# Performance work log

Hardware: AMD Instinct MI355X
Metric: run time of the kernel (lower is better)

Reference implementation:

```python
import jax, jax.numpy as jnp
import numpy as np

DIM = 512
HID = 1024        # dim * expansion_factor
QK = 128          # query_key_dim
G = 256           # group_size
EPS = 1e-5


def setup_inputs() -> dict:
    key = jax.random.key(0)
    ks = jax.random.split(key, 6)
    x = jax.random.normal(ks[0], (4, 4096, DIM), jnp.float32)
    ln_w = jnp.ones((DIM,), jnp.float32)
    ln_b = jnp.zeros((DIM,), jnp.float32)
    Wh = 0.02 * jax.random.normal(ks[1], (DIM, 2 * HID), jnp.float32)
    bh = jnp.zeros((2 * HID,), jnp.float32)
    Wqk = 0.02 * jax.random.normal(ks[2], (DIM, QK), jnp.float32)
    bqk = jnp.zeros((QK,), jnp.float32)
    gamma = 0.02 * jax.random.normal(ks[3], (4, QK), jnp.float32)  # nn.init.normal_(gamma, std=0.02)
    beta = jnp.zeros((4, QK), jnp.float32)
    Wo = 0.02 * jax.random.normal(ks[4], (HID, DIM), jnp.float32)
    bo = jnp.zeros((DIM,), jnp.float32)
    return {"x": x, "ln_w": ln_w, "ln_b": ln_b, "Wh": Wh, "bh": bh,
            "Wqk": Wqk, "bqk": bqk, "gamma": gamma, "beta": beta,
            "Wo": Wo, "bo": bo}


def reference(x, ln_w, ln_b, Wh, bh, Wqk, bqk, gamma, beta, Wo, bo):
    b, n, _ = x.shape
    g = n // G  # number of groups (n chosen as multiple of G -> no padding)

    # LayerNorm (torch uses biased variance)
    mu = jnp.mean(x, axis=-1, keepdims=True)
    var = jnp.mean((x - mu) ** 2, axis=-1, keepdims=True)
    normed = (x - mu) * jax.lax.rsqrt(var + EPS) * ln_w + ln_b

    # to_hidden: Linear -> SiLU, split into v / gate
    h = jax.nn.silu(normed @ Wh + bh)            # [b, n, 2*HID]
    v, gate = jnp.split(h, 2, axis=-1)           # each [b, n, HID]

    # to_qk: Linear -> SiLU, then 4-head offset/scale
    qk = jax.nn.silu(normed @ Wqk + bqk)         # [b, n, QK]
    qkh = qk[..., None, :] * gamma + beta        # [b, n, 4, QK]
    quad_q, lin_q, quad_k, lin_k = (qkh[..., i, :] for i in range(4))

    # group: b (g n) d -> b g n d
    grp = lambda t: t.reshape(b, g, G, t.shape[-1])
    qq, qk_, lq, lk, vv = map(grp, (quad_q, quad_k, lin_q, lin_k, v))

    # quadratic (group-local) attention with ReLU^2 scores, causal within group
    sim = jnp.einsum('bgid,bgjd->bgij', qq, qk_) / G
    attn = jnp.square(jnp.maximum(sim, 0.0))
    causal_mask = jnp.triu(jnp.ones((G, G), dtype=bool), 1)
    attn = jnp.where(causal_mask, 0.0, attn)
    quad_out = jnp.einsum('bgij,bgje->bgie', attn, vv)   # [b, g, G, HID]

    # linear attention across groups: per-group kv, exclusive cumsum over group dim
    lin_kv = jnp.einsum('bgnd,bgne->bgde', lk, vv) / G   # [b, g, QK, HID]
    lin_kv = jnp.cumsum(lin_kv, axis=1)
    lin_kv = jnp.pad(lin_kv, ((0, 0), (1, 0), (0, 0), (0, 0)))[:, :-1]
    lin_out = jnp.einsum('bgde,bgnd->bgne', lin_kv, lq)  # [b, g, G, HID]

    out = gate * (quad_out.reshape(b, n, HID) + lin_out.reshape(b, n, HID))
    return out @ Wo + bo + x
```

## Files before the change

kernel.cpp:

```cpp
#include <hip/hip_runtime.h>
#include <hip/hip_bf16.h>
#include <math.h>


#define BATCH 4
#define SEQ   4096
#define TROWS 16384
#define DIMD  512
#define HIDD  1024
#define QKD   128
#define GRP   256
#define NGRP  16
#define BGRP  64
#define EPIW  132
#define EPB   130

typedef unsigned short bfraw;
typedef __attribute__((ext_vector_type(8))) short bf16x8;
typedef __attribute__((ext_vector_type(8))) unsigned short u16x8;
typedef __attribute__((ext_vector_type(4))) unsigned int u32x4;
typedef __attribute__((ext_vector_type(4))) float f32x4;

__device__ __forceinline__ float bf2f(bfraw u) {
    union { float f; unsigned int i; } c;
    c.i = ((unsigned int)u) << 16;
    return c.f;
}
__device__ __forceinline__ bfraw f2bf(float f) {
    unsigned int x = __float_as_uint(f);
    unsigned int r = (x + 0x7fffu + ((x >> 16) & 1u)) >> 16;
    return (bfraw)r;
}
__device__ __forceinline__ unsigned int pkbf(float lo, float hi) {
    __hip_bfloat162 h2 = __float22bfloat162_rn(make_float2(lo, hi));
    union { __hip_bfloat162 h; unsigned int u; } c; c.h = h2;
    return c.u;
}
__device__ __forceinline__ void store16bf(bfraw* dst, const float* src) {
    u32x4 a, b;
    #pragma unroll
    for (int k = 0; k < 4; ++k) a[k] = pkbf(src[2 * k], src[2 * k + 1]);
    #pragma unroll
    for (int k = 0; k < 4; ++k) b[k] = pkbf(src[8 + 2 * k], src[8 + 2 * k + 1]);
    *(u32x4*)dst = a;
    *(u32x4*)(dst + 8) = b;
}
__device__ __forceinline__ void store8bf(bfraw* dst, const float* src) {
    u32x4 a;
    #pragma unroll
    for (int k = 0; k < 4; ++k) a[k] = pkbf(src[2 * k], src[2 * k + 1]);
    *(u32x4*)dst = a;
}
__device__ __forceinline__ float silu_f(float z) {
    return z / (1.f + __expf(-z));
}
__device__ __forceinline__ void gload_lds16(const void* g, void* l) {
    __builtin_amdgcn_global_load_lds(
        (const __attribute__((address_space(1))) unsigned int*)g,
        (__attribute__((address_space(3))) unsigned int*)l, 16, 0, 0);
}

__device__ __forceinline__ void mfma_step(const bfraw* As, const bfraw* Bs,
                                          f32x4 acc[4][4], int wm, int wn,
                                          int q, int mi) {
    bf16x8 af[4], bfg[4];
    #pragma unroll
    for (int i = 0; i < 4; ++i)
        af[i] = *(const bf16x8*)&As[(size_t)(wm * 64 + i * 16 + mi) * 32 + q * 8];
    #pragma unroll
    for (int j = 0; j < 4; ++j)
        bfg[j] = *(const bf16x8*)&Bs[(size_t)(wn * 64 + j * 16 + mi) * 32 + q * 8];
    #pragma unroll
    for (int i = 0; i < 4; ++i)
        #pragma unroll
        for (int j = 0; j < 4; ++j)
            acc[i][j] = __builtin_amdgcn_mfma_f32_16x16x32_bf16(af[i], bfg[j], acc[i][j], 0, 0, 0);
}

#define SMEMP_DECL                                              \
    __shared__ __align__(16) char smem_[33280];                 \
    bfraw* A0buf = (bfraw*)smem_;                               \
    bfraw* B0buf = (bfraw*)(smem_ + 8192);                      \
    bfraw* A1buf = (bfraw*)(smem_ + 16384);                     \
    bfraw* B1buf = (bfraw*)(smem_ + 24576);

#define PIPE_DSTS                                               \
    bfraw* a0d  = A0buf + wid * 512;                            \
    bfraw* a0d2 = A0buf + 2048 + wid * 512;                     \
    bfraw* b0d  = B0buf + wid * 512;                            \
    bfraw* b0d2 = B0buf + 2048 + wid * 512;                     \
    bfraw* a1d  = A1buf + wid * 512;                            \
    bfraw* a1d2 = A1buf + 2048 + wid * 512;                     \
    bfraw* b1d  = B1buf + wid * 512;                            \
    bfraw* b1d2 = B1buf + 2048 + wid * 512;

#define KLOOP_PRE(Abase, Astr, Bbase, Bstr)                                    \
    const bfraw* pa0 = (Abase) + (size_t)(t >> 2) * (Astr) + (t & 3) * 8;      \
    const bfraw* pa1 = pa0 + (size_t)64 * (Astr);                              \
    const bfraw* pb0 = (Bbase) + (size_t)(t >> 2) * (Bstr) + (t & 3) * 8;      \
    const bfraw* pb1 = pb0 + (size_t)64 * (Bstr);

#define STAGE0                                                                 \
    do { gload_lds16(pa0, a0d); gload_lds16(pa1, a0d2);                        \
         gload_lds16(pb0, b0d); gload_lds16(pb1, b0d2);                        \
         pa0 += 32; pa1 += 32; pb0 += 32; pb1 += 32; } while (0)
#define STAGE1                                                                 \
    do { gload_lds16(pa0, a1d); gload_lds16(pa1, a1d2);                        \
         gload_lds16(pb0, b1d); gload_lds16(pb1, b1d2);                        \
         pa0 += 32; pa1 += 32; pb0 += 32; pb1 += 32; } while (0)

#define PIPE_LOOP(NIT, Abase, Astr, Bbase, Bstr)                               \
    {                                                                          \
        KLOOP_PRE(Abase, Astr, Bbase, Bstr)                                    \
        STAGE0;                                                                \
        for (int it = 0; it < (NIT); it += 2) {                                \
            __syncthreads();                                                   \
            if (it + 1 < (NIT)) STAGE1;                                        \
            mfma_step(A0buf, B0buf, acc, wm, wn, q, mi);                       \
            __syncthreads();                                                   \
            if (it + 2 < (NIT)) STAGE0;                                        \
            if (it + 1 < (NIT))                                                \
                mfma_step(A1buf, B1buf, acc, wm, wn, q, mi);                   \
        }                                                                      \
        __syncthreads();                                                       \
    }

__device__ __forceinline__ int epi_row(int p, int lr) {
    return (lr < 16) ? (p * 16 + lr) : (64 + p * 16 + (lr - 16));
}

__global__ __launch_bounds__(256) void prep_kernel(const float* __restrict__ x,
                                                   const float* __restrict__ lnw,
                                                   const float* __restrict__ lnb,
                                                   const float* __restrict__ Wh,
                                                   const float* __restrict__ Wo,
                                                   const float* __restrict__ Wqk,
                                                   bfraw* __restrict__ normb,
                                                   bfraw* __restrict__ WhT,
                                                   bfraw* __restrict__ WoT,
                                                   bfraw* __restrict__ WqkT) {
    __shared__ float tile[32][33];
    int bid = blockIdx.x;
    int t = threadIdx.x;
    if (bid < 4096) {
        int row  = bid * 4 + (t >> 6);
        int lane = t & 63;
        const float* xr = x + (size_t)row * DIMD;
        float4 v0 = ((const float4*)xr)[lane];
        float4 v1 = ((const float4*)xr)[lane + 64];
        float s  = v0.x + v0.y + v0.z + v0.w + v1.x + v1.y + v1.z + v1.w;
        float ss = v0.x*v0.x + v0.y*v0.y + v0.z*v0.z + v0.w*v0.w
                 + v1.x*v1.x + v1.y*v1.y + v1.z*v1.z + v1.w*v1.w;
        #pragma unroll
        for (int off = 32; off; off >>= 1) {
            s  += __shfl_xor(s, off);
            ss += __shfl_xor(ss, off);
        }
        float mu  = s * (1.f / DIMD);
        float var = ss * (1.f / DIMD) - mu * mu;
        float inv = rsqrtf(var + 1e-5f);
        float4 w0 = ((const float4*)lnw)[lane],  w1 = ((const float4*)lnw)[lane + 64];
        float4 b0 = ((const float4*)lnb)[lane],  b1 = ((const float4*)lnb)[lane + 64];
        unsigned int o0 = pkbf((v0.x - mu) * inv * w0.x + b0.x,
                               (v0.y - mu) * inv * w0.y + b0.y);
        unsigned int o1 = pkbf((v0.z - mu) * inv * w0.z + b0.z,
                               (v0.w - mu) * inv * w0.w + b0.w);
        unsigned int o2 = pkbf((v1.x - mu) * inv * w1.x + b1.x,
                               (v1.y - mu) * inv * w1.y + b1.y);
        unsigned int o3 = pkbf((v1.z - mu) * inv * w1.z + b1.z,
                               (v1.w - mu) * inv * w1.w + b1.w);
        unsigned int* brow = (unsigned int*)(normb + (size_t)row * DIMD);
        ((uint2*)brow)[lane]      = make_uint2(o0, o1);
        ((uint2*)brow)[lane + 64] = make_uint2(o2, o3);
        return;
    }
    bid -= 4096;
    const float* in; bfraw* outp; int R, C, nx;
    if (bid < 1024)      { in = Wh;  outp = WhT;  R = DIMD; C = 2 * HIDD; nx = 64; }
    else if (bid < 1536) { bid -= 1024; in = Wo;  outp = WoT;  R = HIDD; C = DIMD; nx = 16; }
    else                 { bid -= 1536; in = Wqk; outp = WqkT; R = DIMD; C = QKD;  nx = 4; }
    int c0 = (bid % nx) * 32, r0 = (bid / nx) * 32;
    int tr = t >> 3, tc4 = (t & 7) * 4;
    float4 v = *(const float4*)&in[(size_t)(r0 + tr) * C + c0 + tc4];
    tile[tr][tc4 + 0] = v.x; tile[tr][tc4 + 1] = v.y;
    tile[tr][tc4 + 2] = v.z; tile[tr][tc4 + 3] = v.w;
    __syncthreads();
    ushort4 s;
    s.x = f2bf(tile[tc4 + 0][tr]);
    s.y = f2bf(tile[tc4 + 1][tr]);
    s.z = f2bf(tile[tc4 + 2][tr]);
    s.w = f2bf(tile[tc4 + 3][tr]);
    *(ushort4*)&outp[(size_t)(c0 + tr) * R + r0 + tc4] = s;
}

__global__ __launch_bounds__(512, 4) void gemm_h256(
    const bfraw* __restrict__ A,
    const bfraw* __restrict__ WhT,
    const bfraw* __restrict__ WqkT,
    const float* __restrict__ bh,
    const float* __restrict__ bqk,
    const float* __restrict__ gamma,
    const float* __restrict__ beta,
    bfraw* __restrict__ vT,
    bfraw* __restrict__ gate,
    bfraw* __restrict__ qq,
    bfraw* __restrict__ lq,
    bfraw* __restrict__ kk,
    bfraw* __restrict__ lkT) {
    __shared__ __align__(16) char smem_[73728];
    const int t = threadIdx.x;
    const int lane = t & 63, wid = t >> 6;
    const int wm = wid >> 2, wn = wid & 3;
    const int q = lane >> 4, mi = lane & 15;
    int nid = (blockIdx.x & 7) * 144 + (blockIdx.x >> 3);
    const int ct = nid % 9, by = nid / 9;
    const int r0 = by * 128, c0 = ct * 256;
    const int bg = r0 >> 8;
    const int jb0 = r0 & 255;

    const int lslot = (t & 7) ^ ((t >> 3) & 7);
    const int srow  = 2 * (t >> 3) + (lslot >> 2);
    const int skel  = (lslot & 3) * 8;
    const bfraw* Asrc = A + (size_t)(r0 + srow) * DIMD + skel;
    const bfraw* Bsrc0;
    const bfraw* Bsrc1;
    if (ct < 8) {
        Bsrc0 = WhT + (size_t)(c0 + srow) * DIMD + skel;
        Bsrc1 = Bsrc0 + (size_t)128 * DIMD;
    } else {
        Bsrc0 = WqkT + (size_t)srow * DIMD + skel;
        Bsrc1 = Bsrc0;
    }
    const int swz = ((((mi & 1) << 2) | q) ^ ((mi >> 1) & 7)) << 4;
    const int a_off = (wm * 32 + (mi >> 1)) * 128 + swz;
    const int b_off = (wn * 32 + (mi >> 1)) * 128 + swz;

#define GH_STAGE(KT, SLOT)                                                    \
    do {                                                                      \
        char* sb_ = smem_ + (SLOT) * 24576;                                   \
        gload_lds16(Asrc  + (KT) * 32, sb_ + t * 16);                         \
        gload_lds16(Bsrc0 + (KT) * 32, sb_ + 8192 + t * 16);                  \
        gload_lds16(Bsrc1 + (KT) * 32, sb_ + 16384 + t * 16);                 \
    } while (0)

    f32x4 acc[4][4] = {};
    GH_STAGE(0, 0);
    GH_STAGE(1, 1);
    asm volatile("s_waitcnt vmcnt(3)" ::: "memory");
    __builtin_amdgcn_s_barrier();

    #pragma unroll
    for (int j = 0; j < 16; ++j) {
        if (j + 2 < 16) GH_STAGE(j + 2, (j + 2) % 3);
        const char* cb = smem_ + (j % 3) * 24576;
        bf16x8 af[4], bfr[4];
        #pragma unroll
        for (int mf = 0; mf < 4; ++mf)
            af[mf] = *(const bf16x8*)(cb + a_off + mf * 1024);
        #pragma unroll
        for (int nf = 0; nf < 4; ++nf)
            bfr[nf] = *(const bf16x8*)(cb + 8192 + b_off + nf * 1024);
        __builtin_amdgcn_s_setprio(1);
        #pragma unroll
        for (int mf = 0; mf < 4; ++mf)
            #pragma unroll
            for (int nf = 0; nf < 4; ++nf)
                acc[mf][nf] = __builtin_amdgcn_mfma_f32_16x16x32_bf16(
                    af[mf], bfr[nf], acc[mf][nf], 0, 0, 0);
        __builtin_amdgcn_s_setprio(0);
        if (j + 2 < 16)      asm volatile("s_waitcnt vmcnt(3)" ::: "memory");
        else if (j + 1 < 16) asm volatile("s_waitcnt vmcnt(0)" ::: "memory");
        __builtin_amdgcn_s_barrier();
    }
#undef GH_STAGE

    float* epi = (float*)smem_;
    if (ct == 8) {
        float* gbl = (float*)(smem_ + 36864);
        gbl[t] = gamma[t];
        gbl[t + 512] = beta[t];
        float bq4[4];
        #pragma unroll
        for (int nf = 0; nf < 4; ++nf)
            bq4[nf] = (wn < 2) ? bqk[wn * 64 + nf * 16 + mi] : 0.f;
        #pragma unroll
        for (int p2 = 0; p2 < 4; ++p2) {
            if (wm == (p2 >> 1) && wn < 2) {
                #pragma unroll
                for (int mf2 = 0; mf2 < 2; ++mf2) {
                    int mf = ((p2 & 1) << 1) + mf2;
                    #pragma unroll
                    for (int nf = 0; nf < 4; ++nf)
                        #pragma unroll
                        for (int rg = 0; rg < 4; ++rg)
                            epi[(mf2 * 16 + q * 4 + rg) * 132 + wn * 64 + nf * 16 + mi] =
                                silu_f(acc[mf][nf][rg] + bq4[nf]);
                }
            }
            __syncthreads();
            {
                int lr = t >> 4, cs = (t & 15) * 8;
                float z[8];
                #pragma unroll
                for (int k = 0; k < 8; ++k) z[k] = epi[lr * 132 + cs + k];
                size_t growr = (size_t)(r0 + p2 * 32 + lr) * QKD + cs;
                #pragma unroll
                for (int hd = 0; hd < 3; ++hd) {
                    bfraw* arr = (hd == 0) ? qq : (hd == 1) ? lq : kk;
                    float tmp[8];
                    #pragma unroll
                    for (int k = 0; k < 8; ++k)
                        tmp[k] = z[k] * gbl[hd * 128 + cs + k] + gbl[512 + hd * 128 + cs + k];
                    store8bf(arr + growr, tmp);
                }
            }
            {
                int c = t >> 2, jh = (t & 3) * 8;
                float g3 = gbl[384 + c], e3 = gbl[896 + c];
                float tmp[8];
                #pragma unroll
                for (int k = 0; k < 8; ++k)
                    tmp[k] = epi[(jh + k) * 132 + c] * g3 + e3;
                store8bf(lkT + ((size_t)bg * QKD + c) * GRP + jb0 + p2 * 32 + jh, tmp);
            }
            __syncthreads();
        }
        return;
    }
    float bias4[4];
    #pragma unroll
    for (int nf = 0; nf < 4; ++nf)
        bias4[nf] = bh[c0 + wn * 64 + nf * 16 + mi];
    if (ct < 4) {
        #pragma unroll
        for (int p2 = 0; p2 < 4; ++p2) {
            if (wm == (p2 >> 1)) {
                #pragma unroll
                for (int mf2 = 0; mf2 < 2; ++mf2) {
                    int mf = ((p2 & 1) << 1) + mf2;
                    #pragma unroll
                    for (int nf = 0; nf < 4; ++nf)
                        #pragma unroll
                        for (int rg = 0; rg < 4; ++rg)
                            epi[(mf2 * 16 + q * 4 + rg) * 257 + wn * 64 + nf * 16 + mi] =
                                silu_f(acc[mf][nf][rg] + bias4[nf]);
                }
            }
            __syncthreads();
            int e2 = t >> 1, js = (t & 1) * 16;
            float tmp[16];
            #pragma unroll
            for (int k = 0; k < 16; ++k)
                tmp[k] = epi[(js + k) * 257 + e2];
            store16bf(vT + ((size_t)bg * HIDD + c0 + e2) * GRP + jb0 + p2 * 32 + js, tmp);
            __syncthreads();
        }
    } else {
        #pragma unroll
        for (int p2 = 0; p2 < 4; ++p2) {
            if (wm == (p2 >> 1)) {
                #pragma unroll
                for (int mf2 = 0; mf2 < 2; ++mf2) {
                    int mf = ((p2 & 1) << 1) + mf2;
                    #pragma unroll
                    for (int nf = 0; nf < 4; ++nf)
                        #pragma unroll
                        for (int rg = 0; rg < 4; ++rg)
                            epi[(mf2 * 16 + q * 4 + rg) * 260 + wn * 64 + nf * 16 + mi] =
                                silu_f(acc[mf][nf][rg] + bias4[nf]);
                }
            }
            __syncthreads();
            int lr = t >> 4, cs = (t & 15) * 16;
            float tmp[16];
            #pragma unroll
            for (int k = 0; k < 16; ++k)
                tmp[k] = epi[lr * 260 + cs + k];
            store16bf(gate + (size_t)(r0 + p2 * 32 + lr) * HIDD + (c0 - HIDD) + cs, tmp);
            __syncthreads();
        }
    }
}

__global__ __launch_bounds__(256) void simkv_kernel(const bfraw* __restrict__ qq,
                                                    const bfraw* __restrict__ kk,
                                                    bfraw* __restrict__ attn,
                                                    const bfraw* __restrict__ vT,
                                                    const bfraw* __restrict__ lkT,
                                                    bfraw* __restrict__ kvT_raw) {
    SMEMP_DECL
    float* epi = (float*)smem_;
    int t = threadIdx.x;
    int lane = t & 63, wid = t >> 6;
    int wm = wid >> 1, wn = wid & 1;
    int q = lane >> 4, mi = lane & 15;
    int bid = blockIdx.x;
    f32x4 acc[4][4] = {};
    PIPE_DSTS
    if (bid < 512) {
        int bg = bid >> 3;
        int row0 = (bid & 7) * 128;
        PIPE_LOOP(8, vT + (size_t)bg * HIDD * GRP + (size_t)row0 * GRP, GRP,
                  lkT + (size_t)bg * QKD * GRP, GRP)
        bfraw* outg = kvT_raw + (size_t)bg * HIDD * QKD;
        #pragma unroll
        for (int p = 0; p < 4; ++p) {
            #pragma unroll
            for (int j = 0; j < 4; ++j)
                #pragma unroll
                for (int rg = 0; rg < 4; ++rg)
                    epi[(wm * 16 + q * 4 + rg) * EPIW + wn * 64 + j * 16 + mi] = acc[p][j][rg];
            __syncthreads();
            int lr = t >> 3, c0t = (t & 7) * 16;
            int gr = row0 + epi_row(p, lr);
            store16bf(outg + (size_t)gr * QKD + c0t, &epi[lr * EPIW + c0t]);
            __syncthreads();
        }
        return;
    }
    int i = bid - 512;
    int bg = i & 63;
    int tid = i >> 6;
    int ry = (tid == 0) ? 0 : 1;
    int rx = (tid == 2) ? 1 : 0;
    int row0 = ry * 128, col0 = rx * 128;
    PIPE_LOOP(4, qq + (size_t)(bg * GRP + row0) * QKD, QKD,
              kk + (size_t)(bg * GRP + col0) * QKD, QKD)
    bfraw* ag = attn + (size_t)bg * GRP * GRP;
    #pragma unroll
    for (int p = 0; p < 4; ++p) {
        #pragma unroll
        for (int j = 0; j < 4; ++j) {
            int colg = col0 + wn * 64 + j * 16 + mi;
            #pragma unroll
            for (int rg = 0; rg < 4; ++rg) {
                int rowg = row0 + wm * 64 + p * 16 + q * 4 + rg;
                float s = acc[p][j][rg] * (1.f / GRP);
                s = fmaxf(s, 0.f);
                s = s * s;
                epi[(wm * 16 + q * 4 + rg) * EPIW + wn * 64 + j * 16 + mi] =
                    (colg > rowg) ? 0.f : s;
            }
        }
        __syncthreads();
        int lr = t >> 3, c0t = (t & 7) * 16;
        int gr = row0 + epi_row(p, lr);
        store16bf(ag + (size_t)gr * GRP + col0 + c0t, &epi[lr * EPIW + c0t]);
        __syncthreads();
    }
}

__global__ __launch_bounds__(256) void cumsum2_kernel(const bfraw* __restrict__ raw,
                                                      bfraw* __restrict__ ex) {
    int idx = blockIdx.x * 256 + threadIdx.x;
    int b = idx >> 17;
    int r = idx & 131071;
    const bfraw* rp = raw + (size_t)b * NGRP * 131072 + r;
    bfraw* ep = ex + (size_t)b * NGRP * 131072 + r;
    float run = 0.f;
    #pragma unroll
    for (int g = 0; g < NGRP; ++g) {
        ep[(size_t)g * 131072] = f2bf(run);
        run += bf2f(rp[(size_t)g * 131072]) * (1.f / GRP);
    }
}

__global__ __launch_bounds__(512, 4) void quadlin256(
    const bfraw* __restrict__ attn,
    const bfraw* __restrict__ vT,
    const bfraw* __restrict__ lq,
    const bfraw* __restrict__ kvT_ex,
    const bfraw* __restrict__ gate,
    bfraw* __restrict__ gated) {
    __shared__ __align__(16) char smem_[73728];
    const int t = threadIdx.x;
    const int lane = t & 63, wid = t >> 6;
    const int wm = wid >> 2, wn = wid & 3;
    const int q = lane >> 4, mi = lane & 15;
    int nid = (blockIdx.x & 7) * 64 + (blockIdx.x >> 3);
    const int bg = nid >> 3;
    const int row0 = ((nid >> 2) & 1) * 128;
    const int c0 = (nid & 3) * 256;

    const int lslot = (t & 7) ^ ((t >> 3) & 7);
    const int srow  = 2 * (t >> 3) + (lslot >> 2);
    const int skel  = (lslot & 3) * 8;
    const bfraw* A1 = attn + ((size_t)bg * GRP + row0 + srow) * GRP + skel;
    const bfraw* B1a = vT + ((size_t)bg * HIDD + c0 + srow) * GRP + skel;
    const bfraw* B1b = B1a + (size_t)128 * GRP;
    const bfraw* A2 = lq + ((size_t)bg * GRP + row0 + srow) * QKD + skel;
    const bfraw* B2a = kvT_ex + ((size_t)bg * HIDD + c0 + srow) * QKD + skel;
    const bfraw* B2b = B2a + (size_t)128 * QKD;

    const int swz = ((((mi & 1) << 2) | q) ^ ((mi >> 1) & 7)) << 4;
    const int a_off = (wm * 32 + (mi >> 1)) * 128 + swz;
    const int b_off = (wn * 32 + (mi >> 1)) * 128 + swz;

#define QL_STAGE(PA, PB0, PB1, KT, SLOT)                                      \
    do {                                                                      \
        char* sb_ = smem_ + (SLOT) * 24576;                                   \
        gload_lds16((PA)  + (KT) * 32, sb_ + t * 16);                         \
        gload_lds16((PB0) + (KT) * 32, sb_ + 8192 + t * 16);                  \
        gload_lds16((PB1) + (KT) * 32, sb_ + 16384 + t * 16);                 \
    } while (0)
#define QL_MFMA(SLOT)                                                         \
    do {                                                                      \
        const char* cb = smem_ + (SLOT) * 24576;                              \
        bf16x8 af[4], bfr[4];                                                 \
        _Pragma("unroll")                                                     \
        for (int mf = 0; mf < 4; ++mf)                                        \
            af[mf] = *(const bf16x8*)(cb + a_off + mf * 1024);                \
        _Pragma("unroll")                                                     \
        for (int nf = 0; nf < 4; ++nf)                                        \
            bfr[nf] = *(const bf16x8*)(cb + 8192 + b_off + nf * 1024);        \
        __builtin_amdgcn_s_setprio(1);                                        \
        _Pragma("unroll")                                                     \
        for (int mf = 0; mf < 4; ++mf)                                        \
            _Pragma("unroll")                                                 \
            for (int nf = 0; nf < 4; ++nf)                                    \
                acc[mf][nf] = __builtin_amdgcn_mfma_f32_16x16x32_bf16(        \
                    af[mf], bfr[nf], acc[mf][nf], 0, 0, 0);                   \
        __builtin_amdgcn_s_setprio(0);                                        \
    } while (0)

    f32x4 acc[4][4] = {};
    const int nit1 = (row0 + 128) >> 5;
    QL_STAGE(A1, B1a, B1b, 0, 0);
    QL_STAGE(A1, B1a, B1b, 1, 1);
    asm volatile("s_waitcnt vmcnt(3)" ::: "memory");
    __builtin_amdgcn_s_barrier();
    for (int j = 0; j < nit1; ++j) {
        if (j + 2 < nit1) QL_STAGE(A1, B1a, B1b, j + 2, (j + 2) % 3);
        QL_MFMA(j % 3);
        if (j + 2 < nit1)      asm volatile("s_waitcnt vmcnt(3)" ::: "memory");
        else if (j + 1 < nit1) asm volatile("s_waitcnt vmcnt(0)" ::: "memory");
        __builtin_amdgcn_s_barrier();
    }
    QL_STAGE(A2, B2a, B2b, 0, 0);
    QL_STAGE(A2, B2a, B2b, 1, 1);
    asm volatile("s_waitcnt vmcnt(3)" ::: "memory");
    __builtin_amdgcn_s_barrier();
    #pragma unroll
    for (int j = 0; j < 4; ++j) {
        if (j + 2 < 4) QL_STAGE(A2, B2a, B2b, j + 2, (j + 2) % 3);
        QL_MFMA(j % 3);
        if (j + 2 < 4)      asm volatile("s_waitcnt vmcnt(3)" ::: "memory");
        else if (j + 1 < 4) asm volatile("s_waitcnt vmcnt(0)" ::: "memory");
        __builtin_amdgcn_s_barrier();
    }
#undef QL_STAGE
#undef QL_MFMA

    float* epi = (float*)smem_;
    #pragma unroll
    for (int p2 = 0; p2 < 4; ++p2) {
        if (wm == (p2 >> 1)) {
            #pragma unroll
            for (int mf2 = 0; mf2 < 2; ++mf2) {
                int mf = ((p2 & 1) << 1) + mf2;
                #pragma unroll
                for (int nf = 0; nf < 4; ++nf)
                    #pragma unroll
                    for (int rg = 0; rg < 4; ++rg)
                        epi[(mf2 * 16 + q * 4 + rg) * 260 + wn * 64 + nf * 16 + mi] =
                            acc[mf][nf][rg];
            }
        }
        __syncthreads();
        int lr = t >> 4, cs = (t & 15) * 16;
        size_t grow = (size_t)bg * GRP + row0 + p2 * 32 + lr;
        const float* src = epi + lr * 260 + cs;
        const bfraw* gsrc = gate + grow * HIDD + c0 + cs;
        u16x8 g0 = *(const u16x8*)gsrc;
        u16x8 g1 = *(const u16x8*)(gsrc + 8);
        float tmp[16];
        #pragma unroll
        for (int k = 0; k < 8; ++k) tmp[k] = src[k] * bf2f(g0[k]);
        #pragma unroll
        for (int k = 0; k < 8; ++k) tmp[8 + k] = src[8 + k] * bf2f(g1[k]);
        store16bf(gated + grow * HIDD + c0 + cs, tmp);
        __syncthreads();
    }
}

__global__ __launch_bounds__(1024, 4) void gemm_final(
    const bfraw* __restrict__ A,
    const bfraw* __restrict__ BT,
    const float* __restrict__ bo,
    const float* __restrict__ x,
    float* __restrict__ out) {
    __shared__ __align__(16) char smem_[147456];
    const int t = threadIdx.x;
    const int lane = t & 63, wid = t >> 6;
    const int wm = wid >> 2, wn = wid & 3;
    const int q = lane >> 4, mi = lane & 15;
    int nid = (blockIdx.x & 7) * 32 + (blockIdx.x >> 3);
    const int by = nid >> 2, cx = nid & 3;
    const int r0 = by * 256, c0 = cx * 128;

    const int lslot = (t & 7) ^ ((t >> 3) & 7);
    const int a_row = 2 * (t >> 3) + (lslot >> 2);
    const int a_kel = (lslot & 3) * 8;
    const bfraw* Asrc = A + (size_t)(r0 + a_row) * HIDD + a_kel;
    const int u = t & 511;
    const int lsb = (u & 7) ^ ((u >> 3) & 7);
    const int b_row = 2 * (u >> 3) + (lsb >> 2);
    const int b_kel = (lsb & 3) * 8 + (t >> 9) * 32;
    const bfraw* Bsrc = BT + (size_t)(c0 + b_row) * HIDD + b_kel;

    const int swz = ((((mi & 1) << 2) | q) ^ ((mi >> 1) & 7)) << 4;
    const int a_off = (wm * 32 + (mi >> 1)) * 128 + swz;
    const int b_off = (wn * 16 + (mi >> 1)) * 128 + swz;

#define GF_STAGE(SS, SLOT)                                                    \
    do {                                                                      \
        char* sb_ = smem_ + (SLOT) * 49152;                                   \
        gload_lds16(Asrc + (SS) * 64,      sb_ + t * 16);                     \
        gload_lds16(Asrc + (SS) * 64 + 32, sb_ + 16384 + t * 16);             \
        gload_lds16(Bsrc + (SS) * 64,      sb_ + 32768 + t * 16);             \
    } while (0)

    f32x4 acc[4][2] = {};
    GF_STAGE(0, 0);
    GF_STAGE(1, 1);
    asm volatile("s_waitcnt vmcnt(3)" ::: "memory");
    __builtin_amdgcn_s_barrier();

    #pragma unroll
    for (int ss = 0; ss < 16; ++ss) {
        if (ss + 2 < 16) GF_STAGE(ss + 2, (ss + 2) % 3);
        const char* cb = smem_ + (ss % 3) * 49152;
        #pragma unroll
        for (int h = 0; h < 2; ++h) {
            bf16x8 af[4], bfr[2];
            #pragma unroll
            for (int mf = 0; mf < 4; ++mf)
                af[mf] = *(const bf16x8*)(cb + h * 16384 + a_off + mf * 1024);
            #pragma unroll
            for (int nf = 0; nf < 2; ++nf)
                bfr[nf] = *(const bf16x8*)(cb + 32768 + h * 8192 + b_off + nf * 1024);
            __builtin_amdgcn_s_setprio(1);
            #pragma unroll
            for (int mf = 0; mf < 4; ++mf)
                #pragma unroll
                for (int nf = 0; nf < 2; ++nf)
                    acc[mf][nf] = __builtin_amdgcn_mfma_f32_16x16x32_bf16(
                        af[mf], bfr[nf], acc[mf][nf], 0, 0, 0);
            __builtin_amdgcn_s_setprio(0);
        }
        if (ss + 2 < 16)      asm volatile("s_waitcnt vmcnt(3)" ::: "memory");
        else if (ss + 1 < 16) asm volatile("s_waitcnt vmcnt(0)" ::: "memory");
        __builtin_amdgcn_s_barrier();
    }
#undef GF_STAGE

    float* epi = (float*)smem_;
    float bo2[2];
    #pragma unroll
    for (int nf = 0; nf < 2; ++nf)
        bo2[nf] = bo[c0 + wn * 32 + nf * 16 + mi];
    #pragma unroll
    for (int p = 0; p < 4; ++p) {
        if (wm == p) {
            #pragma unroll
            for (int mf = 0; mf < 4; ++mf)
                #pragma unroll
                for (int nf = 0; nf < 2; ++nf)
                    #pragma unroll
                    for (int rg = 0; rg < 4; ++rg)
                        epi[(mf * 16 + q * 4 + rg) * 132 + wn * 32 + nf * 16 + mi] =
                            acc[mf][nf][rg] + bo2[nf];
        }
        __syncthreads();
        int lr = t >> 4, cs = (t & 15) * 8;
        const float* src = epi + lr * 132 + cs;
        const float* xs = x + (size_t)(r0 + p * 64 + lr) * DIMD + c0 + cs;
        float* dst = out + (size_t)(r0 + p * 64 + lr) * DIMD + c0 + cs;
        #pragma unroll
        for (int v = 0; v < 2; ++v) {
            float4 a = ((const float4*)src)[v];
            float4 xv = ((const float4*)xs)[v];
            a.x += xv.x; a.y += xv.y; a.z += xv.z; a.w += xv.w;
            ((float4*)dst)[v] = a;
        }
        __syncthreads();
    }
}

extern "C" void kernel_launch(void* const* d_in, const int* in_sizes, int n_in,
                              void* d_out, int out_size, void* d_ws, size_t ws_size,
                              hipStream_t stream) {
    const float* x     = (const float*)d_in[0];
    const float* ln_w  = (const float*)d_in[1];
    const float* ln_b  = (const float*)d_in[2];
    const float* Wh    = (const float*)d_in[3];
    const float* bh    = (const float*)d_in[4];
    const float* Wqk   = (const float*)d_in[5];
    const float* bqk   = (const float*)d_in[6];
    const float* gamma = (const float*)d_in[7];
    const float* beta  = (const float*)d_in[8];
    const float* Wo    = (const float*)d_in[9];
    const float* bo    = (const float*)d_in[10];
    float* out = (float*)d_out;

    char* outb_ = (char*)d_out;
    bfraw* attn = (bfraw*)(outb_);
    bfraw* qq   = (bfraw*)(outb_ + 8388608);
    bfraw* kk   = (bfraw*)(outb_ + 12582912);
    bfraw* lq   = (bfraw*)(outb_ + 16777216);
    bfraw* WhT  = (bfraw*)(outb_ + 20971520);
    bfraw* WqkT = (bfraw*)(outb_ + 23068672);

    char* wsb = (char*)d_ws;
    bfraw* vT      = (bfraw*)(wsb);
    bfraw* gate    = (bfraw*)(wsb + 33554432);
    bfraw* gated   = (bfraw*)(wsb + 67108864);
    bfraw* normb   = (bfraw*)(wsb + 100663296);
    bfraw* kvT_raw = (bfraw*)(wsb + 117440512);
    bfraw* kvT_ex  = (bfraw*)(wsb + 134217728);
    bfraw* lkT     = (bfraw*)(wsb + 150994944);
    bfraw* WoT     = (bfraw*)(wsb + 155189248);

    prep_kernel<<<4096 + 1024 + 512 + 64, 256, 0, stream>>>(
        x, ln_w, ln_b, Wh, Wo, Wqk, normb, WhT, WoT, WqkT);
    gemm_h256<<<1152, 512, 0, stream>>>(
        normb, WhT, WqkT, bh, bqk, gamma, beta, vT, gate, qq, lq, kk, lkT);
    simkv_kernel<<<512 + 192, 256, 0, stream>>>(qq, kk, attn, vT, lkT, kvT_raw);
    cumsum2_kernel<<<(BATCH * QKD * HIDD) / 256, 256, 0, stream>>>(kvT_raw, kvT_ex);
    quadlin256<<<512, 512, 0, stream>>>(attn, vT, lq, kvT_ex, gate, gated);
    gemm_final<<<256, 1024, 0, stream>>>(gated, WoT, bo, x, out);
}
```

Measured before the change: 240.4 us.

## Rewrite simkv as 256-wide tiles with triple-buffered swizzled LDS pipeline

Replaces the 256-thread simkv kernel, which used 128x128 tiles and a double-buffered pipeline, with a 512-thread kernel. Each block now computes a 256x128 (kv) or 128x256 (sim) tile, so 384 blocks replace 704. The new pipeline keeps three LDS stages with explicit vmcnt waits, uses an XOR-swizzled LDS layout to avoid bank conflicts, raises wave priority around the MFMAs, and remaps block ids across XCDs. The sim blocks now cover each full row strip, so they also compute the fully masked upper tiles that the old code skipped.

```diff
diff --git a/kernel.cpp b/kernel.cpp
--- a/kernel.cpp
+++ b/kernel.cpp
@@ -12,8 +12,6 @@
 #define GRP   256
 #define NGRP  16
 #define BGRP  64
-#define EPIW  132
-#define EPB   130
 
 typedef unsigned short bfraw;
 typedef __attribute__((ext_vector_type(8))) short bf16x8;
@@ -58,75 +56,6 @@
     __builtin_amdgcn_global_load_lds(
         (const __attribute__((address_space(1))) unsigned int*)g,
         (__attribute__((address_space(3))) unsigned int*)l, 16, 0, 0);
-}
-
-__device__ __forceinline__ void mfma_step(const bfraw* As, const bfraw* Bs,
-                                          f32x4 acc[4][4], int wm, int wn,
-                                          int q, int mi) {
-    bf16x8 af[4], bfg[4];
-    #pragma unroll
-    for (int i = 0; i < 4; ++i)
-        af[i] = *(const bf16x8*)&As[(size_t)(wm * 64 + i * 16 + mi) * 32 + q * 8];
-    #pragma unroll
-    for (int j = 0; j < 4; ++j)
-        bfg[j] = *(const bf16x8*)&Bs[(size_t)(wn * 64 + j * 16 + mi) * 32 + q * 8];
-    #pragma unroll
-    for (int i = 0; i < 4; ++i)
-        #pragma unroll
-        for (int j = 0; j < 4; ++j)
-            acc[i][j] = __builtin_amdgcn_mfma_f32_16x16x32_bf16(af[i], bfg[j], acc[i][j], 0, 0, 0);
-}
-
-#define SMEMP_DECL                                              \
-    __shared__ __align__(16) char smem_[33280];                 \
-    bfraw* A0buf = (bfraw*)smem_;                               \
-    bfraw* B0buf = (bfraw*)(smem_ + 8192);                      \
-    bfraw* A1buf = (bfraw*)(smem_ + 16384);                     \
-    bfraw* B1buf = (bfraw*)(smem_ + 24576);
-
-#define PIPE_DSTS                                               \
-    bfraw* a0d  = A0buf + wid * 512;                            \
-    bfraw* a0d2 = A0buf + 2048 + wid * 512;                     \
-    bfraw* b0d  = B0buf + wid * 512;                            \
-    bfraw* b0d2 = B0buf + 2048 + wid * 512;                     \
-    bfraw* a1d  = A1buf + wid * 512;                            \
-    bfraw* a1d2 = A1buf + 2048 + wid * 512;                     \
-    bfraw* b1d  = B1buf + wid * 512;                            \
-    bfraw* b1d2 = B1buf + 2048 + wid * 512;
-
-#define KLOOP_PRE(Abase, Astr, Bbase, Bstr)                                    \
-    const bfraw* pa0 = (Abase) + (size_t)(t >> 2) * (Astr) + (t & 3) * 8;      \
-    const bfraw* pa1 = pa0 + (size_t)64 * (Astr);                              \
-    const bfraw* pb0 = (Bbase) + (size_t)(t >> 2) * (Bstr) + (t & 3) * 8;      \
-    const bfraw* pb1 = pb0 + (size_t)64 * (Bstr);
-
-#define STAGE0                                                                 \
-    do { gload_lds16(pa0, a0d); gload_lds16(pa1, a0d2);                        \
-         gload_lds16(pb0, b0d); gload_lds16(pb1, b0d2);                        \
-         pa0 += 32; pa1 += 32; pb0 += 32; pb1 += 32; } while (0)
-#define STAGE1                                                                 \
-    do { gload_lds16(pa0, a1d); gload_lds16(pa1, a1d2);                        \
-         gload_lds16(pb0, b1d); gload_lds16(pb1, b1d2);                        \
-         pa0 += 32; pa1 += 32; pb0 += 32; pb1 += 32; } while (0)
-
-#define PIPE_LOOP(NIT, Abase, Astr, Bbase, Bstr)                               \
-    {                                                                          \
-        KLOOP_PRE(Abase, Astr, Bbase, Bstr)                                    \
-        STAGE0;                                                                \
-        for (int it = 0; it < (NIT); it += 2) {                                \
-            __syncthreads();                                                   \
-            if (it + 1 < (NIT)) STAGE1;                                        \
-            mfma_step(A0buf, B0buf, acc, wm, wn, q, mi);                       \
-            __syncthreads();                                                   \
-            if (it + 2 < (NIT)) STAGE0;                                        \
-            if (it + 1 < (NIT))                                                \
-                mfma_step(A1buf, B1buf, acc, wm, wn, q, mi);                   \
-        }                                                                      \
-        __syncthreads();                                                       \
-    }
-
-__device__ __forceinline__ int epi_row(int p, int lr) {
-    return (lr < 16) ? (p * 16 + lr) : (64 + p * 16 + (lr - 16));
 }
 
 __global__ __launch_bounds__(256) void prep_kernel(const float* __restrict__ x,
@@ -382,70 +311,158 @@
     }
 }
 
-__global__ __launch_bounds__(256) void simkv_kernel(const bfraw* __restrict__ qq,
-                                                    const bfraw* __restrict__ kk,
-                                                    bfraw* __restrict__ attn,
-                                                    const bfraw* __restrict__ vT,
-                                                    const bfraw* __restrict__ lkT,
-                                                    bfraw* __restrict__ kvT_raw) {
-    SMEMP_DECL
+__global__ __launch_bounds__(512, 4) void simkv256(
+    const bfraw* __restrict__ qq,
+    const bfraw* __restrict__ kk,
+    bfraw* __restrict__ attn,
+    const bfraw* __restrict__ vT,
+    const bfraw* __restrict__ lkT,
+    bfraw* __restrict__ kvT_raw) {
+    __shared__ __align__(16) char smem_[73728];
+    const int t = threadIdx.x;
+    const int lane = t & 63, wid = t >> 6;
+    const int q = lane >> 4, mi = lane & 15;
+    int nid = (blockIdx.x & 7) * 48 + (blockIdx.x >> 3);
+    const int lslot = (t & 7) ^ ((t >> 3) & 7);
+    const int srow  = 2 * (t >> 3) + (lslot >> 2);
+    const int skel  = (lslot & 3) * 8;
+    const int swz = ((((mi & 1) << 2) | q) ^ ((mi >> 1) & 7)) << 4;
+    f32x4 acc[4][4] = {};
     float* epi = (float*)smem_;
-    int t = threadIdx.x;
-    int lane = t & 63, wid = t >> 6;
-    int wm = wid >> 1, wn = wid & 1;
-    int q = lane >> 4, mi = lane & 15;
-    int bid = blockIdx.x;
-    f32x4 acc[4][4] = {};
-    PIPE_DSTS
-    if (bid < 512) {
-        int bg = bid >> 3;
-        int row0 = (bid & 7) * 128;
-        PIPE_LOOP(8, vT + (size_t)bg * HIDD * GRP + (size_t)row0 * GRP, GRP,
-                  lkT + (size_t)bg * QKD * GRP, GRP)
-        bfraw* outg = kvT_raw + (size_t)bg * HIDD * QKD;
+
+    if (nid < 256) {
+        const int bg = nid >> 2, e0 = (nid & 3) * 256;
+        const int wmE = wid >> 1, wnD = wid & 1;
+        const bfraw* Bsrc  = lkT + ((size_t)bg * QKD + srow) * GRP + skel;
+        const bfraw* Asrc0 = vT + ((size_t)bg * HIDD + e0 + srow) * GRP + skel;
+        const bfraw* Asrc1 = Asrc0 + (size_t)128 * GRP;
+        const int a_off = (wmE * 32 + (mi >> 1)) * 128 + swz;
+        const int b_off = (wnD * 32 + (mi >> 1)) * 128 + swz;
+#define KV_STAGE(KT, SLOT)                                                    \
+    do {                                                                      \
+        char* sb_ = smem_ + (SLOT) * 24576;                                   \
+        gload_lds16(Bsrc  + (KT) * 32, sb_ + t * 16);                         \
+        gload_lds16(Asrc0 + (KT) * 32, sb_ + 8192 + t * 16);                  \
+        gload_lds16(Asrc1 + (KT) * 32, sb_ + 16384 + t * 16);                 \
+    } while (0)
+        KV_STAGE(0, 0);
+        KV_STAGE(1, 1);
+        asm volatile("s_waitcnt vmcnt(3)" ::: "memory");
+        __builtin_amdgcn_s_barrier();
+        #pragma unroll
+        for (int j = 0; j < 8; ++j) {
+            if (j + 2 < 8) KV_STAGE(j + 2, (j + 2) % 3);
+            const char* cb = smem_ + (j % 3) * 24576;
+            bf16x8 af[4], bfr[4];
+            #pragma unroll
+            for (int mf = 0; mf < 4; ++mf)
+                af[mf] = *(const bf16x8*)(cb + 8192 + a_off + mf * 1024);
+            #pragma unroll
+            for (int nf = 0; nf < 4; ++nf)
+                bfr[nf] = *(const bf16x8*)(cb + b_off + nf * 1024);
+            __builtin_amdgcn_s_setprio(1);
+            #pragma unroll
+            for (int mf = 0; mf < 4; ++mf)
+                #pragma unroll
+                for (int nf = 0; nf < 4; ++nf)
+                    acc[mf][nf] = __builtin_amdgcn_mfma_f32_16x16x32_bf16(
+                        af[mf], bfr[nf], acc[mf][nf], 0, 0, 0);
+            __builtin_amdgcn_s_setprio(0);
+            if (j + 2 < 8)      asm volatile("s_waitcnt vmcnt(3)" ::: "memory");
+            else if (j + 1 < 8) asm volatile("s_waitcnt vmcnt(0)" ::: "memory");
+            __builtin_amdgcn_s_barrier();
+        }
+#undef KV_STAGE
         #pragma unroll
         for (int p = 0; p < 4; ++p) {
-            #pragma unroll
-            for (int j = 0; j < 4; ++j)
-                #pragma unroll
-                for (int rg = 0; rg < 4; ++rg)
-                    epi[(wm * 16 + q * 4 + rg) * EPIW + wn * 64 + j * 16 + mi] = acc[p][j][rg];
+            if (wmE == p) {
+                #pragma unroll
+                for (int mf = 0; mf < 4; ++mf)
+                    #pragma unroll
+                    for (int nf = 0; nf < 4; ++nf)
+                        #pragma unroll
+                        for (int rg = 0; rg < 4; ++rg)
+                            epi[(mf * 16 + q * 4 + rg) * 132 + wnD * 64 + nf * 16 + mi] =
+                                acc[mf][nf][rg];
+            }
             __syncthreads();
-            int lr = t >> 3, c0t = (t & 7) * 16;
-            int gr = row0 + epi_row(p, lr);
-            store16bf(outg + (size_t)gr * QKD + c0t, &epi[lr * EPIW + c0t]);
+            int lr = t >> 3, cs = (t & 7) * 16;
+            store16bf(kvT_raw + ((size_t)bg * HIDD + e0 + p * 64 + lr) * QKD + cs,
+                      &epi[lr * 132 + cs]);
             __syncthreads();
         }
         return;
     }
-    int i = bid - 512;
-    int bg = i & 63;
-    int tid = i >> 6;
-    int ry = (tid == 0) ? 0 : 1;
-    int rx = (tid == 2) ? 1 : 0;
-    int row0 = ry * 128, col0 = rx * 128;
-    PIPE_LOOP(4, qq + (size_t)(bg * GRP + row0) * QKD, QKD,
-              kk + (size_t)(bg * GRP + col0) * QKD, QKD)
-    bfraw* ag = attn + (size_t)bg * GRP * GRP;
-    #pragma unroll
-    for (int p = 0; p < 4; ++p) {
-        #pragma unroll
-        for (int j = 0; j < 4; ++j) {
-            int colg = col0 + wn * 64 + j * 16 + mi;
-            #pragma unroll
-            for (int rg = 0; rg < 4; ++rg) {
-                int rowg = row0 + wm * 64 + p * 16 + q * 4 + rg;
-                float s = acc[p][j][rg] * (1.f / GRP);
-                s = fmaxf(s, 0.f);
-                s = s * s;
-                epi[(wm * 16 + q * 4 + rg) * EPIW + wn * 64 + j * 16 + mi] =
-                    (colg > rowg) ? 0.f : s;
+    int s = nid - 256;
+    const int bg = s >> 1, row0 = (s & 1) * 128;
+    const int wm = wid >> 2, wn = wid & 3;
+    const bfraw* Asrc  = qq + ((size_t)bg * GRP + row0 + srow) * QKD + skel;
+    const bfraw* Bsrc0 = kk + ((size_t)bg * GRP + srow) * QKD + skel;
+    const bfraw* Bsrc1 = Bsrc0 + (size_t)128 * QKD;
+    const int a_off = (wm * 32 + (mi >> 1)) * 128 + swz;
+    const int b_off = (wn * 32 + (mi >> 1)) * 128 + swz;
+#define SM_STAGE(KT, SLOT)                                                    \
+    do {                                                                      \
+        char* sb_ = smem_ + (SLOT) * 24576;                                   \
+        gload_lds16(Asrc  + (KT) * 32, sb_ + t * 16);                         \
+        gload_lds16(Bsrc0 + (KT) * 32, sb_ + 8192 + t * 16);                  \
+        gload_lds16(Bsrc1 + (KT) * 32, sb_ + 16384 + t * 16);                 \
+    } while (0)
+    SM_STAGE(0, 0);
+    SM_STAGE(1, 1);
+    asm volatile("s_waitcnt vmcnt(3)" ::: "memory");
+    __builtin_amdgcn_s_barrier();
+    #pragma unroll
+    for (int j = 0; j < 4; ++j) {
+        if (j + 2 < 4) SM_STAGE(j + 2, (j + 2) % 3);
+        const char* cb = smem_ + (j % 3) * 24576;
+        bf16x8 af[4], bfr[4];
+        #pragma unroll
+        for (int mf = 0; mf < 4; ++mf)
+            af[mf] = *(const bf16x8*)(cb + a_off + mf * 1024);
+        #pragma unroll
+        for (int nf = 0; nf < 4; ++nf)
+            bfr[nf] = *(const bf16x8*)(cb + 8192 + b_off + nf * 1024);
+        __builtin_amdgcn_s_setprio(1);
+        #pragma unroll
+        for (int mf = 0; mf < 4; ++mf)
+            #pragma unroll
+            for (int nf = 0; nf < 4; ++nf)
+                acc[mf][nf] = __builtin_amdgcn_mfma_f32_16x16x32_bf16(
+                    af[mf], bfr[nf], acc[mf][nf], 0, 0, 0);
+        __builtin_amdgcn_s_setprio(0);
+        if (j + 2 < 4)      asm volatile("s_waitcnt vmcnt(3)" ::: "memory");
+        else if (j + 1 < 4) asm volatile("s_waitcnt vmcnt(0)" ::: "memory");
+        __builtin_amdgcn_s_barrier();
+    }
+#undef SM_STAGE
+    #pragma unroll
+    for (int p2 = 0; p2 < 4; ++p2) {
+        if (wm == (p2 >> 1)) {
+            #pragma unroll
+            for (int mf2 = 0; mf2 < 2; ++mf2) {
+                int mf = ((p2 & 1) << 1) + mf2;
+                #pragma unroll
+                for (int nf = 0; nf < 4; ++nf) {
+                    int colg = wn * 64 + nf * 16 + mi;
+                    #pragma unroll
+                    for (int rg = 0; rg < 4; ++rg) {
+                        int rowg = row0 + p2 * 32 + mf2 * 16 + q * 4 + rg;
+                        float v = acc[mf][nf][rg] * (1.f / GRP);
+                        v = fmaxf(v, 0.f);
+                        v = v * v;
+                        epi[(mf2 * 16 + q * 4 + rg) * 260 + colg] =
+                            (colg > rowg) ? 0.f : v;
+                    }
+                }
             }
         }
         __syncthreads();
-        int lr = t >> 3, c0t = (t & 7) * 16;
-        int gr = row0 + epi_row(p, lr);
-        store16bf(ag + (size_t)gr * GRP + col0 + c0t, &epi[lr * EPIW + c0t]);
+        int lr = t >> 4, cs = (t & 15) * 16;
+        float tmp[16];
+        #pragma unroll
+        for (int k = 0; k < 16; ++k) tmp[k] = epi[lr * 260 + cs + k];
+        store16bf(attn + ((size_t)bg * GRP + row0 + p2 * 32 + lr) * GRP + cs, tmp);
         __syncthreads();
     }
 }
@@ -725,7 +742,7 @@
         x, ln_w, ln_b, Wh, Wo, Wqk, normb, WhT, WoT, WqkT);
     gemm_h256<<<1152, 512, 0, stream>>>(
         normb, WhT, WqkT, bh, bqk, gamma, beta, vT, gate, qq, lq, kk, lkT);
-    simkv_kernel<<<512 + 192, 256, 0, stream>>>(qq, kk, attn, vT, lkT, kvT_raw);
+    simkv256<<<384, 512, 0, stream>>>(qq, kk, attn, vT, lkT, kvT_raw);
     cumsum2_kernel<<<(BATCH * QKD * HIDD) / 256, 256, 0, stream>>>(kvT_raw, kvT_ex);
     quadlin256<<<512, 512, 0, stream>>>(attn, vT, lq, kvT_ex, gate, gated);
     gemm_final<<<256, 1024, 0, stream>>>(gated, WoT, bo, x, out);
```

Result: slower. 245.3 us (+2.0%).
